# Kernel tuning notes

Hardware: AMD Instinct MI355X
Metric: run time of the kernel (lower is better)

## Reference

```python
import jax, jax.numpy as jnp
import numpy as np
from jax import lax

K = 5        # kernel size
STRIDE = 1
DN = ('NCHW', 'OIHW', 'NCHW')


def _dist_conv(x, w):
    """Euclidean distance between every kxk window of x [B,1,H,W] and each
    filter w [O,1,k,k] -> [B,O,Hout,Wout].  Uses the identity
    ||p - w||^2 = sum(p^2) - 2 p.w + ||w||^2 so the cross term is one conv."""
    xw = lax.conv_general_dilated(x, w, (STRIDE, STRIDE), 'VALID',
                                  dimension_numbers=DN)
    ones = jnp.ones((1, 1, K, K), x.dtype)
    x2 = lax.conv_general_dilated(x * x, ones, (STRIDE, STRIDE), 'VALID',
                                  dimension_numbers=DN)
    w2 = jnp.sum(w * w, axis=(1, 2, 3))[None, :, None, None]
    d2 = jnp.maximum(x2 - 2.0 * xw + w2, 1e-12)  # clamp for sqrt stability
    return jnp.sqrt(d2)


def setup_inputs() -> dict:
    key = jax.random.key(0)
    k1, k2, k3, k4 = jax.random.split(key, 4)
    B, H, W, O = 16, 112, 112, 256
    gray_input = jax.random.normal(k1, (B, 1, H, W), jnp.float32)
    rgb_input = jax.random.normal(k2, (B, 1, H, W), jnp.float32)
    # kaiming-uniform-like init, first filter zeroed (as in reset_parameters)
    bound = 1.0 / np.sqrt(K * K)
    gray_weight = jax.random.uniform(k3, (O, 1, K, K), jnp.float32, -bound, bound)
    gray_weight = gray_weight.at[0].set(0.0)
    rgb_weight = jax.random.uniform(k4, (O, 1, K, K), jnp.float32, -bound, bound)
    rgb_weight = rgb_weight.at[0].set(0.0)
    std = jnp.asarray(2.0, jnp.float32)
    return {"gray_input": gray_input, "rgb_input": rgb_input,
            "gray_weight": gray_weight, "rgb_weight": rgb_weight, "std": std}


def reference(gray_input, rgb_input, gray_weight, rgb_weight, std):
    d = _dist_conv(gray_input, gray_weight) + _dist_conv(rgb_input, rgb_weight)
    # gaussian RBF on the summed distances
    return jnp.exp(-(d * d) / (2.0 * std * std))
```

## Files before the change

### kernel.cpp

```cpp
#include <hip/hip_runtime.h>
#include <math.h>

#define BB    16
#define HH    112
#define IMSZ  (HH*HH)
#define OO    256
#define OHW   108
#define PLANE (OHW*OHW)
#define MTOTAL (BB*PLANE)
#define MTILE 256
#define KSUB  3
#define WRECB 144
#define WRECW 36
#define NXCD  8

typedef __attribute__((ext_vector_type(8))) short short8;
typedef __attribute__((ext_vector_type(4))) float f32x4;

__device__ __forceinline__ unsigned short f2bf(float x) {
    unsigned u = __builtin_bit_cast(unsigned, x);
    return (unsigned short)((u + 0x7fffu + ((u >> 16) & 1u)) >> 16);
}
__device__ __forceinline__ float bf2f(unsigned short h) {
    unsigned u = ((unsigned)h) << 16;
    return __builtin_bit_cast(float, u);
}

__global__ __launch_bounds__(1024)
void dist_rbf_mfma(const float* __restrict__ gx, const float* __restrict__ rx,
                   const float* __restrict__ gw, const float* __restrict__ rw,
                   const float* __restrict__ stdp, float* __restrict__ out)
{
    __shared__ __align__(16) unsigned wrec[2 * OO * WRECW];
    __shared__ float w2s[2 * OO];

    const int tid = threadIdx.x;

    const int nwg = gridDim.x;
    const int hw  = blockIdx.x;
    const int xcd = hw % NXCD, idx = hw / NXCD;
    const int q = nwg / NXCD, r = nwg % NXCD;
    const int lb = (xcd < r ? xcd * (q + 1) : r * (q + 1) + (xcd - r) * q) + idx;

    if (tid < 2 * OO) {
        const int img = tid >> 8;
        const int o   = tid & 255;
        const float* wsrc = img ? rw : gw;
        unsigned* rec = wrec + img * OO * WRECW + o * WRECW;
        float v[32]; unsigned short h[32];
        float s = 0.f;
        #pragma unroll
        for (int i = 0; i < 32; i++) {
            float x = (i < 25) ? wsrc[o * 25 + i] : 0.f;
            v[i] = x; s = fmaf(x, x, s); h[i] = f2bf(x);
        }
        w2s[img * OO + o] = s;
        #pragma unroll
        for (int wd = 0; wd < 16; wd++) {
            rec[wd] = (unsigned)h[2*wd] | ((unsigned)h[2*wd+1] << 16);
            unsigned short l0 = f2bf(v[2*wd]   - bf2f(h[2*wd]));
            unsigned short l1 = f2bf(v[2*wd+1] - bf2f(h[2*wd+1]));
            rec[16 + wd] = (unsigned)l0 | ((unsigned)l1 << 16);
        }
    }
    __syncthreads();

    const int lid  = tid & 63;
    const int wid  = tid >> 6;
    const int mcol = lid & 15;
    const int kgrp = lid >> 4;
    const int k0   = kgrp * 8;

    const float sd   = stdp[0];
    const float kneg = -1.f / (2.f * sd * sd);
    const char* wrecB = (const char*)wrec;

    for (int st = 0; st < KSUB; st++) {
        const int pbase = (lb * KSUB + st) * MTILE;

        short8 ah[2], al[2];
        float  x2v[2][4];

        {
            const int p  = pbase + wid * 16 + mcol;
            const int b  = p / PLANE;
            const int pp = p - b * PLANE;
            const int oh = pp / OHW;
            const int ow = pp - oh * OHW;
            const size_t ibase = (size_t)b * IMSZ + oh * HH + ow;
            #pragma unroll
            for (int img = 0; img < 2; img++) {
                const float* src = (img == 0 ? gx : rx) + ibase;
                float xs[8];
                float part = 0.f;
                #pragma unroll
                for (int j = 0; j < 8; j++) {
                    int k = k0 + j;
                    int r2 = k / 5, c2 = k - r2 * 5;
                    float x = (k < 25) ? src[r2 * HH + c2] : 0.f;
                    xs[j] = x; part = fmaf(x, x, part);
                }
                part += __shfl_xor(part, 16);
                part += __shfl_xor(part, 32);
                #pragma unroll
                for (int rr = 0; rr < 4; rr++)
                    x2v[img][rr] = __shfl(part, kgrp * 4 + rr);
                short8 hi, lo;
                #pragma unroll
                for (int j = 0; j < 8; j++) {
                    unsigned short hh = f2bf(xs[j]);
                    hi[j] = (short)hh;
                    lo[j] = (short)f2bf(xs[j] - bf2f(hh));
                }
                ah[img] = hi; al[img] = lo;
            }
        }

        #pragma unroll 2
        for (int ot = 0; ot < 16; ot++) {
            const int o = ot * 16 + mcol;
            const char* recg = wrecB + (size_t)o * WRECB + kgrp * 16;
            const char* recr = recg + (size_t)OO * WRECB;
            short8 bhg = *(const short8*)recg;
            short8 blg = *(const short8*)(recg + 64);
            short8 bhr = *(const short8*)recr;
            short8 blr = *(const short8*)(recr + 64);
            const float w2g = w2s[o];
            const float w2r = w2s[OO + o];

            f32x4 cg = {0.f, 0.f, 0.f, 0.f};
            f32x4 cr = {0.f, 0.f, 0.f, 0.f};
            cg = __builtin_amdgcn_mfma_f32_16x16x32_bf16(ah[0], bhg, cg, 0, 0, 0);
            cg = __builtin_amdgcn_mfma_f32_16x16x32_bf16(ah[0], blg, cg, 0, 0, 0);
            cg = __builtin_amdgcn_mfma_f32_16x16x32_bf16(al[0], bhg, cg, 0, 0, 0);
            cr = __builtin_amdgcn_mfma_f32_16x16x32_bf16(ah[1], bhr, cr, 0, 0, 0);
            cr = __builtin_amdgcn_mfma_f32_16x16x32_bf16(ah[1], blr, cr, 0, 0, 0);
            cr = __builtin_amdgcn_mfma_f32_16x16x32_bf16(al[1], bhr, cr, 0, 0, 0);

            f32x4 res;
            #pragma unroll
            for (int rr = 0; rr < 4; rr++) {
                float d2g = fmaf(-2.f, cg[rr], x2v[0][rr] + w2g);
                float d2r = fmaf(-2.f, cr[rr], x2v[1][rr] + w2r);
                d2g = fmaxf(d2g, 1e-12f);
                d2r = fmaxf(d2r, 1e-12f);
                float d2 = fmaf(2.f, __builtin_amdgcn_sqrtf(d2g * d2r), d2g + d2r);
                res[rr] = __expf(kneg * d2);
            }
            const int prow0 = pbase + wid * 16 + kgrp * 4;
            const int b0  = prow0 / PLANE;
            const int pp0 = prow0 - b0 * PLANE;
            *(f32x4*)(out + ((size_t)(b0 * OO + o)) * PLANE + pp0) = res;
        }
    }
}

extern "C" void kernel_launch(void* const* d_in, const int* in_sizes, int n_in,
                              void* d_out, int out_size, void* d_ws, size_t ws_size,
                              hipStream_t stream) {
    const float* gx   = (const float*)d_in[0];
    const float* rx   = (const float*)d_in[1];
    const float* gw   = (const float*)d_in[2];
    const float* rw   = (const float*)d_in[3];
    const float* stdp = (const float*)d_in[4];
    float* out = (float*)d_out;

    dim3 grid(MTOTAL / (MTILE * KSUB), 1, 1);
    dim3 block(1024, 1, 1);
    dist_rbf_mfma<<<grid, block, 0, stream>>>(gx, rx, gw, rw, stdp, out);
}
```

Measured before the change: 46.66 us.

## Load all sub-tile activations upfront and reuse weight fragments across sub-tiles

Activation fragments for all three M sub-tiles are now gathered and converted before the output-channel loop. The loop is inverted so each weight fragment read from LDS serves three sub-tiles instead of one. This cuts LDS weight reads by three times and issues all global input loads at once to overlap their latency. In exchange, register pressure rises from holding the A fragments and x2 values for three sub-tiles, which at 1024 threads per block could cause spills.

```diff
diff --git a/kernel.cpp b/kernel.cpp
--- a/kernel.cpp
+++ b/kernel.cpp
@@ -75,82 +75,84 @@
     const float kneg = -1.f / (2.f * sd * sd);
     const char* wrecB = (const char*)wrec;
 
+    short8 ah[KSUB][2], al[KSUB][2];
+    float  x2v[KSUB][2][4];
+    float* outbase[KSUB];
+
+    #pragma unroll
     for (int st = 0; st < KSUB; st++) {
         const int pbase = (lb * KSUB + st) * MTILE;
+        const int p  = pbase + wid * 16 + mcol;
+        const int b  = p / PLANE;
+        const int pp = p - b * PLANE;
+        const int oh = pp / OHW;
+        const int ow = pp - oh * OHW;
+        const size_t ibase = (size_t)b * IMSZ + oh * HH + ow;
+        #pragma unroll
+        for (int img = 0; img < 2; img++) {
+            const float* src = (img == 0 ? gx : rx) + ibase;
+            float xs[8];
+            float part = 0.f;
+            #pragma unroll
+            for (int j = 0; j < 8; j++) {
+                int k = k0 + j;
+                int r2 = k / 5, c2 = k - r2 * 5;
+                float x = (k < 25) ? src[r2 * HH + c2] : 0.f;
+                xs[j] = x; part = fmaf(x, x, part);
+            }
+            part += __shfl_xor(part, 16);
+            part += __shfl_xor(part, 32);
+            #pragma unroll
+            for (int rr = 0; rr < 4; rr++)
+                x2v[st][img][rr] = __shfl(part, kgrp * 4 + rr);
+            short8 hi, lo;
+            #pragma unroll
+            for (int j = 0; j < 8; j++) {
+                unsigned short hh = f2bf(xs[j]);
+                hi[j] = (short)hh;
+                lo[j] = (short)f2bf(xs[j] - bf2f(hh));
+            }
+            ah[st][img] = hi; al[st][img] = lo;
+        }
+        const int prow0 = pbase + wid * 16 + kgrp * 4;
+        const int b0  = prow0 / PLANE;
+        const int pp0 = prow0 - b0 * PLANE;
+        outbase[st] = out + (size_t)b0 * OO * PLANE + pp0;
+    }
 
-        short8 ah[2], al[2];
-        float  x2v[2][4];
+    for (int ot = 0; ot < 16; ot++) {
+        const int o = ot * 16 + mcol;
+        const char* recg = wrecB + (size_t)o * WRECB + kgrp * 16;
+        const char* recr = recg + (size_t)OO * WRECB;
+        short8 bhg = *(const short8*)recg;
+        short8 blg = *(const short8*)(recg + 64);
+        short8 bhr = *(const short8*)recr;
+        short8 blr = *(const short8*)(recr + 64);
+        const float w2g = w2s[o];
+        const float w2r = w2s[OO + o];
 
-        {
-            const int p  = pbase + wid * 16 + mcol;
-            const int b  = p / PLANE;
-            const int pp = p - b * PLANE;
-            const int oh = pp / OHW;
-            const int ow = pp - oh * OHW;
-            const size_t ibase = (size_t)b * IMSZ + oh * HH + ow;
-            #pragma unroll
-            for (int img = 0; img < 2; img++) {
-                const float* src = (img == 0 ? gx : rx) + ibase;
-                float xs[8];
-                float part = 0.f;
-                #pragma unroll
-                for (int j = 0; j < 8; j++) {
-                    int k = k0 + j;
-                    int r2 = k / 5, c2 = k - r2 * 5;
-                    float x = (k < 25) ? src[r2 * HH + c2] : 0.f;
-                    xs[j] = x; part = fmaf(x, x, part);
-                }
-                part += __shfl_xor(part, 16);
-                part += __shfl_xor(part, 32);
-                #pragma unroll
-                for (int rr = 0; rr < 4; rr++)
-                    x2v[img][rr] = __shfl(part, kgrp * 4 + rr);
-                short8 hi, lo;
-                #pragma unroll
-                for (int j = 0; j < 8; j++) {
-                    unsigned short hh = f2bf(xs[j]);
-                    hi[j] = (short)hh;
-                    lo[j] = (short)f2bf(xs[j] - bf2f(hh));
-                }
-                ah[img] = hi; al[img] = lo;
-            }
-        }
-
-        #pragma unroll 2
-        for (int ot = 0; ot < 16; ot++) {
-            const int o = ot * 16 + mcol;
-            const char* recg = wrecB + (size_t)o * WRECB + kgrp * 16;
-            const char* recr = recg + (size_t)OO * WRECB;
-            short8 bhg = *(const short8*)recg;
-            short8 blg = *(const short8*)(recg + 64);
-            short8 bhr = *(const short8*)recr;
-            short8 blr = *(const short8*)(recr + 64);
-            const float w2g = w2s[o];
-            const float w2r = w2s[OO + o];
-
+        #pragma unroll
+        for (int st = 0; st < KSUB; st++) {
             f32x4 cg = {0.f, 0.f, 0.f, 0.f};
             f32x4 cr = {0.f, 0.f, 0.f, 0.f};
-            cg = __builtin_amdgcn_mfma_f32_16x16x32_bf16(ah[0], bhg, cg, 0, 0, 0);
-            cg = __builtin_amdgcn_mfma_f32_16x16x32_bf16(ah[0], blg, cg, 0, 0, 0);
-            cg = __builtin_amdgcn_mfma_f32_16x16x32_bf16(al[0], bhg, cg, 0, 0, 0);
-            cr = __builtin_amdgcn_mfma_f32_16x16x32_bf16(ah[1], bhr, cr, 0, 0, 0);
-            cr = __builtin_amdgcn_mfma_f32_16x16x32_bf16(ah[1], blr, cr, 0, 0, 0);
-            cr = __builtin_amdgcn_mfma_f32_16x16x32_bf16(al[1], bhr, cr, 0, 0, 0);
+            cg = __builtin_amdgcn_mfma_f32_16x16x32_bf16(ah[st][0], bhg, cg, 0, 0, 0);
+            cg = __builtin_amdgcn_mfma_f32_16x16x32_bf16(ah[st][0], blg, cg, 0, 0, 0);
+            cg = __builtin_amdgcn_mfma_f32_16x16x32_bf16(al[st][0], bhg, cg, 0, 0, 0);
+            cr = __builtin_amdgcn_mfma_f32_16x16x32_bf16(ah[st][1], bhr, cr, 0, 0, 0);
+            cr = __builtin_amdgcn_mfma_f32_16x16x32_bf16(ah[st][1], blr, cr, 0, 0, 0);
+            cr = __builtin_amdgcn_mfma_f32_16x16x32_bf16(al[st][1], bhr, cr, 0, 0, 0);
 
             f32x4 res;
             #pragma unroll
             for (int rr = 0; rr < 4; rr++) {
-                float d2g = fmaf(-2.f, cg[rr], x2v[0][rr] + w2g);
-                float d2r = fmaf(-2.f, cr[rr], x2v[1][rr] + w2r);
+                float d2g = fmaf(-2.f, cg[rr], x2v[st][0][rr] + w2g);
+                float d2r = fmaf(-2.f, cr[rr], x2v[st][1][rr] + w2r);
                 d2g = fmaxf(d2g, 1e-12f);
                 d2r = fmaxf(d2r, 1e-12f);
                 float d2 = fmaf(2.f, __builtin_amdgcn_sqrtf(d2g * d2r), d2g + d2r);
                 res[rr] = __expf(kneg * d2);
             }
-            const int prow0 = pbase + wid * 16 + kgrp * 4;
-            const int b0  = prow0 / PLANE;
-            const int pp0 = prow0 - b0 * PLANE;
-            *(f32x4*)(out + ((size_t)(b0 * OO + o)) * PLANE + pp0) = res;
+            *(f32x4*)(outbase[st] + (size_t)o * PLANE) = res;
         }
     }
 }
```

Measured after the change: 46.71 us. Within noise of the previous version (+0.1%).

## Retile work by batch and 16-channel output tile, keep weights in registers

Applied to the files above, without the earlier changes.

The grid changes from pixel tiles spanning all 256 output channels to one block per (batch, 16-channel tile). Each block loops over every pixel fragment of its plane. Weight fragments now load once into registers instead of being read from LDS per channel tile, and output writes become contiguous runs within a single channel plane. The cost is that input patches are re-read from global memory (through cache) 16 times per batch, once per channel tile, instead of once.

```diff
diff --git a/kernel.cpp b/kernel.cpp
--- a/kernel.cpp
+++ b/kernel.cpp
@@ -5,11 +5,10 @@
 #define HH    112
 #define IMSZ  (HH*HH)
 #define OO    256
+#define OTILE 16
 #define OHW   108
 #define PLANE (OHW*OHW)
-#define MTOTAL (BB*PLANE)
-#define MTILE 256
-#define KSUB  3
+#define NFRAG (PLANE/16)
 #define WRECB 144
 #define WRECW 36
 #define NXCD  8
@@ -31,30 +30,28 @@
                    const float* __restrict__ gw, const float* __restrict__ rw,
                    const float* __restrict__ stdp, float* __restrict__ out)
 {
-    __shared__ __align__(16) unsigned wrec[2 * OO * WRECW];
-    __shared__ float w2s[2 * OO];
+    __shared__ __align__(16) unsigned wrec[2 * OTILE * WRECW];
+    __shared__ float w2s[2 * OTILE];
 
     const int tid = threadIdx.x;
 
-    const int nwg = gridDim.x;
-    const int hw  = blockIdx.x;
-    const int xcd = hw % NXCD, idx = hw / NXCD;
-    const int q = nwg / NXCD, r = nwg % NXCD;
-    const int lb = (xcd < r ? xcd * (q + 1) : r * (q + 1) + (xcd - r) * q) + idx;
+    const int lbk   = (blockIdx.x & (NXCD - 1)) * (256 / NXCD) + (blockIdx.x >> 3);
+    const int b     = lbk >> 4;
+    const int obase = (lbk & 15) * OTILE;
 
-    if (tid < 2 * OO) {
-        const int img = tid >> 8;
-        const int o   = tid & 255;
-        const float* wsrc = img ? rw : gw;
-        unsigned* rec = wrec + img * OO * WRECW + o * WRECW;
+    if (tid < 2 * OTILE) {
+        const int img = tid >> 4;
+        const int ol  = tid & 15;
+        const float* wsrc = (img ? rw : gw) + (size_t)(obase + ol) * 25;
+        unsigned* rec = wrec + (img * OTILE + ol) * WRECW;
         float v[32]; unsigned short h[32];
         float s = 0.f;
         #pragma unroll
         for (int i = 0; i < 32; i++) {
-            float x = (i < 25) ? wsrc[o * 25 + i] : 0.f;
+            float x = (i < 25) ? wsrc[i] : 0.f;
             v[i] = x; s = fmaf(x, x, s); h[i] = f2bf(x);
         }
-        w2s[img * OO + o] = s;
+        w2s[img * OTILE + ol] = s;
         #pragma unroll
         for (int wd = 0; wd < 16; wd++) {
             rec[wd] = (unsigned)h[2*wd] | ((unsigned)h[2*wd+1] << 16);
@@ -73,85 +70,76 @@
 
     const float sd   = stdp[0];
     const float kneg = -1.f / (2.f * sd * sd);
+
     const char* wrecB = (const char*)wrec;
+    const char* recg = wrecB + (size_t)mcol * WRECB + kgrp * 16;
+    const char* recr = recg + (size_t)OTILE * WRECB;
+    const short8 bhg = *(const short8*)recg;
+    const short8 blg = *(const short8*)(recg + 64);
+    const short8 bhr = *(const short8*)recr;
+    const short8 blr = *(const short8*)(recr + 64);
+    const float  w2g = w2s[mcol];
+    const float  w2r = w2s[OTILE + mcol];
 
-    for (int st = 0; st < KSUB; st++) {
-        const int pbase = (lb * KSUB + st) * MTILE;
+    const float* gsrc = gx + (size_t)b * IMSZ;
+    const float* rsrc = rx + (size_t)b * IMSZ;
+    float* outp = out + ((size_t)(b * OO + obase + mcol)) * PLANE;
+
+    for (int f = wid; f < NFRAG; f += 16) {
+        const int p  = f * 16 + mcol;
+        const int oh = p / OHW;
+        const int ow = p - oh * OHW;
+        const size_t ibase = (size_t)oh * HH + ow;
 
         short8 ah[2], al[2];
         float  x2v[2][4];
-
-        {
-            const int p  = pbase + wid * 16 + mcol;
-            const int b  = p / PLANE;
-            const int pp = p - b * PLANE;
-            const int oh = pp / OHW;
-            const int ow = pp - oh * OHW;
-            const size_t ibase = (size_t)b * IMSZ + oh * HH + ow;
+        #pragma unroll
+        for (int img = 0; img < 2; img++) {
+            const float* src = (img == 0 ? gsrc : rsrc) + ibase;
+            float xs[8];
+            float part = 0.f;
             #pragma unroll
-            for (int img = 0; img < 2; img++) {
-                const float* src = (img == 0 ? gx : rx) + ibase;
-                float xs[8];
-                float part = 0.f;
-                #pragma unroll
-                for (int j = 0; j < 8; j++) {
-                    int k = k0 + j;
-                    int r2 = k / 5, c2 = k - r2 * 5;
-                    float x = (k < 25) ? src[r2 * HH + c2] : 0.f;
-                    xs[j] = x; part = fmaf(x, x, part);
-                }
-                part += __shfl_xor(part, 16);
-                part += __shfl_xor(part, 32);
-                #pragma unroll
-                for (int rr = 0; rr < 4; rr++)
-                    x2v[img][rr] = __shfl(part, kgrp * 4 + rr);
-                short8 hi, lo;
-                #pragma unroll
-                for (int j = 0; j < 8; j++) {
-                    unsigned short hh = f2bf(xs[j]);
-                    hi[j] = (short)hh;
-                    lo[j] = (short)f2bf(xs[j] - bf2f(hh));
-                }
-                ah[img] = hi; al[img] = lo;
+            for (int j = 0; j < 8; j++) {
+                int k = k0 + j;
+                int r2 = k / 5, c2 = k - r2 * 5;
+                float x = (k < 25) ? src[r2 * HH + c2] : 0.f;
+                xs[j] = x; part = fmaf(x, x, part);
             }
+            part += __shfl_xor(part, 16);
+            part += __shfl_xor(part, 32);
+            #pragma unroll
+            for (int rr = 0; rr < 4; rr++)
+                x2v[img][rr] = __shfl(part, kgrp * 4 + rr);
+            short8 hi, lo;
+            #pragma unroll
+            for (int j = 0; j < 8; j++) {
+                unsigned short hh = f2bf(xs[j]);
+                hi[j] = (short)hh;
+                lo[j] = (short)f2bf(xs[j] - bf2f(hh));
+            }
+            ah[img] = hi; al[img] = lo;
         }
 
-        #pragma unroll 2
-        for (int ot = 0; ot < 16; ot++) {
-            const int o = ot * 16 + mcol;
-            const char* recg = wrecB + (size_t)o * WRECB + kgrp * 16;
-            const char* recr = recg + (size_t)OO * WRECB;
-            short8 bhg = *(const short8*)recg;
-            short8 blg = *(const short8*)(recg + 64);
-            short8 bhr = *(const short8*)recr;
-            short8 blr = *(const short8*)(recr + 64);
-            const float w2g = w2s[o];
-            const float w2r = w2s[OO + o];
+        f32x4 cg = {0.f, 0.f, 0.f, 0.f};
+        f32x4 cr = {0.f, 0.f, 0.f, 0.f};
+        cg = __builtin_amdgcn_mfma_f32_16x16x32_bf16(ah[0], bhg, cg, 0, 0, 0);
+        cg = __builtin_amdgcn_mfma_f32_16x16x32_bf16(ah[0], blg, cg, 0, 0, 0);
+        cg = __builtin_amdgcn_mfma_f32_16x16x32_bf16(al[0], bhg, cg, 0, 0, 0);
+        cr = __builtin_amdgcn_mfma_f32_16x16x32_bf16(ah[1], bhr, cr, 0, 0, 0);
+        cr = __builtin_amdgcn_mfma_f32_16x16x32_bf16(ah[1], blr, cr, 0, 0, 0);
+        cr = __builtin_amdgcn_mfma_f32_16x16x32_bf16(al[1], bhr, cr, 0, 0, 0);
 
-            f32x4 cg = {0.f, 0.f, 0.f, 0.f};
-            f32x4 cr = {0.f, 0.f, 0.f, 0.f};
-            cg = __builtin_amdgcn_mfma_f32_16x16x32_bf16(ah[0], bhg, cg, 0, 0, 0);
-            cg = __builtin_amdgcn_mfma_f32_16x16x32_bf16(ah[0], blg, cg, 0, 0, 0);
-            cg = __builtin_amdgcn_mfma_f32_16x16x32_bf16(al[0], bhg, cg, 0, 0, 0);
-            cr = __builtin_amdgcn_mfma_f32_16x16x32_bf16(ah[1], bhr, cr, 0, 0, 0);
-            cr = __builtin_amdgcn_mfma_f32_16x16x32_bf16(ah[1], blr, cr, 0, 0, 0);
-            cr = __builtin_amdgcn_mfma_f32_16x16x32_bf16(al[1], bhr, cr, 0, 0, 0);
-
-            f32x4 res;
-            #pragma unroll
-            for (int rr = 0; rr < 4; rr++) {
-                float d2g = fmaf(-2.f, cg[rr], x2v[0][rr] + w2g);
-                float d2r = fmaf(-2.f, cr[rr], x2v[1][rr] + w2r);
-                d2g = fmaxf(d2g, 1e-12f);
-                d2r = fmaxf(d2r, 1e-12f);
-                float d2 = fmaf(2.f, __builtin_amdgcn_sqrtf(d2g * d2r), d2g + d2r);
-                res[rr] = __expf(kneg * d2);
-            }
-            const int prow0 = pbase + wid * 16 + kgrp * 4;
-            const int b0  = prow0 / PLANE;
-            const int pp0 = prow0 - b0 * PLANE;
-            *(f32x4*)(out + ((size_t)(b0 * OO + o)) * PLANE + pp0) = res;
+        f32x4 res;
+        #pragma unroll
+        for (int rr = 0; rr < 4; rr++) {
+            float d2g = fmaf(-2.f, cg[rr], x2v[0][rr] + w2g);
+            float d2r = fmaf(-2.f, cr[rr], x2v[1][rr] + w2r);
+            d2g = fmaxf(d2g, 1e-12f);
+            d2r = fmaxf(d2r, 1e-12f);
+            float d2 = fmaf(2.f, __builtin_amdgcn_sqrtf(d2g * d2r), d2g + d2r);
+            res[rr] = __expf(kneg * d2);
         }
+        *(f32x4*)(outp + f * 16 + kgrp * 4) = res;
     }
 }
 
@@ -165,7 +153,7 @@
     const float* stdp = (const float*)d_in[4];
     float* out = (float*)d_out;
 
-    dim3 grid(MTOTAL / (MTILE * KSUB), 1, 1);
+    dim3 grid(BB * (OO / OTILE), 1, 1);
     dim3 block(1024, 1, 1);
     dist_rbf_mfma<<<grid, block, 0, stream>>>(gx, rx, gw, rw, stdp, out);
 }
```

New measurement: 98.61 us. +111.3%, slower.
